# Kernel optimization log

Measured on AMD Instinct MI355X. Metric: run time of the kernel, lower is better.

Reference implementation:

```python
import jax, jax.numpy as jnp
import numpy as np

N_QUBITS = 10
N_LAYERS = 4
OUTPUT = 16
BATCH = 4096
DIM = 2 ** N_QUBITS  # 1024, amplitude-embedding dimension


def setup_inputs() -> dict:
    key = jax.random.key(0)
    k1, k2, k3, k4 = jax.random.split(key, 4)
    X = jax.random.normal(k1, (BATCH, DIM), jnp.float32)
    weights = jax.random.normal(k2, (N_LAYERS, N_QUBITS, 3), jnp.float32)  # StronglyEntanglingLayers params
    W = jax.random.normal(k3, (OUTPUT, N_QUBITS), jnp.float32) / np.sqrt(N_QUBITS)
    b = jax.random.normal(k4, (OUTPUT,), jnp.float32) * 0.01
    return {"X": X, "weights": weights, "W": W, "b": b}


def _rot_matrix(phi, theta, omega):
    # PennyLane Rot(phi, theta, omega) = RZ(omega) @ RY(theta) @ RZ(phi)
    c = jnp.cos(theta / 2).astype(jnp.complex64)
    s = jnp.sin(theta / 2).astype(jnp.complex64)
    a = jnp.exp(-0.5j * (phi + omega)) * c
    bq = -jnp.exp(0.5j * (phi - omega)) * s
    cq = jnp.exp(-0.5j * (phi - omega)) * s
    d = jnp.exp(0.5j * (phi + omega)) * c
    return jnp.stack([jnp.stack([a, bq]), jnp.stack([cq, d])])  # (2,2) complex64


def _apply_1q(state, U, q, n):
    # wire 0 is the most-significant bit (PennyLane default.qubit convention)
    A, B = 2 ** q, 2 ** (n - q - 1)
    s = state.reshape(-1, A, 2, B)
    s = jnp.einsum('ij,bajc->baic', U, s)
    return s.reshape(-1, 2 ** n)


def _cnot(state, c, t, n):
    hi, lo = (c, t) if c < t else (t, c)
    s = state.reshape(-1, 2 ** hi, 2, 2 ** (lo - hi - 1), 2, 2 ** (n - lo - 1))
    if c < t:
        # control axis 2, target axis 4
        s0 = s[:, :, 0]                      # (B, H, M, 2, L)
        s1 = jnp.flip(s[:, :, 1], axis=3)    # flip target where control=1
        s = jnp.stack([s0, s1], axis=2)
    else:
        # control axis 4, target axis 2
        s0 = s[:, :, :, :, 0, :]             # (B, H, 2, M, L)
        s1 = jnp.flip(s[:, :, :, :, 1, :], axis=2)
        s = jnp.stack([s0, s1], axis=4)
    return s.reshape(-1, 2 ** n)


def _circuit(X, weights):
    n = N_QUBITS
    # AmplitudeEmbedding (pad_with=0.0; here input dim == 2**n so just normalize)
    nrm = jnp.linalg.norm(X, axis=-1, keepdims=True)
    state = (X / nrm).astype(jnp.complex64)  # (B, 2**n)
    for l in range(N_LAYERS):
        for q in range(n):
            U = _rot_matrix(weights[l, q, 0], weights[l, q, 1], weights[l, q, 2])
            state = _apply_1q(state, U, q, n)
        r = (l % (n - 1)) + 1  # StronglyEntanglingLayers default imprimitive range
        for q in range(n):
            state = _cnot(state, q, (q + r) % n, n)
    probs = state.real ** 2 + state.imag ** 2  # (B, 2**n)
    # <Z_i> = sum_s probs[s] * (1 - 2*bit_i(s)); wire 0 = MSB
    idx = np.arange(2 ** n)
    bits = (idx[:, None] >> np.arange(n - 1, -1, -1)[None, :]) & 1  # (2**n, n)
    signs = jnp.asarray(1 - 2 * bits, jnp.float32)
    return probs @ signs  # (B, n)


def reference(X, weights, W, b):
    z = _circuit(X, weights)          # (B, n_qubits)
    return z @ W.T + b                # Linear head; nn.Tanh is defined but unused in forward
```

## Files before the change

kernel.cpp:

```cpp
#include <hip/hip_runtime.h>
#include <stdint.h>

#define NQ 10
#define DIMQ 1024
#define BATCH 4096

typedef float f32x2 __attribute__((ext_vector_type(2)));

__global__ __launch_bounds__(64) void prep_g(const float* __restrict__ wts,
                                             float* __restrict__ Gg) {
  int g = threadIdx.x;
  if (g < 40) {
    float phi = wts[g * 3 + 0], th = wts[g * 3 + 1], om = wts[g * 3 + 2];
    float ct = cosf(0.5f * th), s = sinf(0.5f * th);
    float ap = 0.5f * (phi + om), am = 0.5f * (phi - om);
    float cp = cosf(ap), spp = sinf(ap), cm = cosf(am), sm = sinf(am);
    float aR = ct * cp,  aI = -ct * spp;
    float bR = -s * cm,  bI = -s * sm;
    float cR = s * cm,   cI = -s * sm;
    float dR = ct * cp,  dI = ct * spp;
    float* o = Gg + g * 16;
    o[0]  = aR;  o[1]  = aR;  o[2]  = -aI; o[3]  = aI;
    o[4]  = bR;  o[5]  = bR;  o[6]  = -bI; o[7]  = bI;
    o[8]  = cR;  o[9]  = cR;  o[10] = -cI; o[11] = cI;
    o[12] = dR;  o[13] = dR;  o[14] = -dI; o[15] = dI;
  }
}

__host__ __device__ constexpr int cperm_c(int x, int r) {
  for (int q = 0; q < NQ; ++q) {
    const int c = 9 - q;
    int t = c - r; if (t < 0) t += NQ;
    x ^= ((x >> c) & 1) << t;
  }
  return x;
}
constexpr int amask(int q) {
  int a = 0;
  for (int b = 0; b < 6; ++b) a |= ((cperm_c(1 << b, 4) >> (9 - q)) & 1) << b;
  return a;
}
constexpr int mmask(int q) {
  int m = 0;
  for (int b = 0; b < 4; ++b) m |= ((cperm_c(1 << (6 + b), 4) >> (9 - q)) & 1) << b;
  return m;
}

__device__ __forceinline__ f32x2 swapv(f32x2 v) {
  return __builtin_shufflevector(v, v, 1, 0);
}

template<int CTRL>
__device__ __forceinline__ float dpp1(float x) {
  return __int_as_float(
      __builtin_amdgcn_update_dpp(0, __float_as_int(x), CTRL, 0xF, 0xF, true));
}
template<int P>
__device__ __forceinline__ float shufl(float x) {
  if constexpr (P == 0)      return dpp1<0xB1>(x);
  else if constexpr (P == 1) return dpp1<0x4E>(x);
  else if constexpr (P == 2) return dpp1<0x141>(dpp1<0x1B>(x));
  else if constexpr (P == 3) return dpp1<0x140>(dpp1<0x141>(x));
  else return __int_as_float(
      __builtin_amdgcn_ds_swizzle(__float_as_int(x), 0x401F));
}

template<int MT>
__device__ __forceinline__ void rotR(f32x2 (&s)[16], const f32x2* __restrict__ C) {
  const f32x2 C0 = C[0], C1 = C[1], C2 = C[2], C3 = C[3];
  const f32x2 C4 = C[4], C5 = C[5], C6 = C[6], C7 = C[7];
  #pragma unroll
  for (int e0 = 0; e0 < 16; ++e0) {
    if (e0 & MT) continue;
    const int e1 = e0 | MT;
    f32x2 x0 = s[e0], x1 = s[e1], w0 = swapv(x0), w1 = swapv(x1);
    s[e0] = C0 * x0 + C1 * w0 + C2 * x1 + C3 * w1;
    s[e1] = C4 * x0 + C5 * w0 + C6 * x1 + C7 * w1;
  }
}

template<int P>
__device__ __forceinline__ void rotL(f32x2 (&s)[16], const f32x2* __restrict__ C,
                                     int lane) {
  const int L = (lane >> P) & 1;
  const f32x2 A0 = L ? C[6] : C[0], A1 = L ? C[7] : C[1];
  const f32x2 B0 = L ? C[4] : C[2], B1 = L ? C[5] : C[3];
  #pragma unroll
  for (int e = 0; e < 16; ++e) {
    f32x2 o;
    o.x = shufl<P>(s[e].x);
    o.y = shufl<P>(s[e].y);
    s[e] = A0 * s[e] + A1 * swapv(s[e]) + B0 * o + B1 * swapv(o);
  }
}

__device__ __forceinline__ void rot5(f32x2 (&s)[16], const f32x2* __restrict__ C,
                                     int lane) {
  const int L = lane >> 5;
  const f32x2 A0 = L ? C[6] : C[0], A1 = L ? C[7] : C[1];
  const f32x2 B0 = L ? C[4] : C[2], B1 = L ? C[5] : C[3];
  #pragma unroll
  for (int e = 0; e < 16; ++e) {
    unsigned xr = __float_as_uint(s[e].x), xi = __float_as_uint(s[e].y);
    auto rr = __builtin_amdgcn_permlane32_swap(xr, xr, false, false);
    auto ri = __builtin_amdgcn_permlane32_swap(xi, xi, false, false);
    f32x2 o;
    o.x = __uint_as_float(L ? rr[0] : rr[1]);
    o.y = __uint_as_float(L ? ri[0] : ri[1]);
    s[e] = A0 * s[e] + A1 * swapv(s[e]) + B0 * o + B1 * swapv(o);
  }
}

template<int R>
__device__ __forceinline__ void perm_state(f32x2 (&s)[16], f32x2* __restrict__ L,
                                           int lane) {
  constexpr int K0=cperm_c(1,R),  K1=cperm_c(2,R),  K2=cperm_c(4,R),
                K3=cperm_c(8,R),  K4=cperm_c(16,R), K5=cperm_c(32,R),
                C6=cperm_c(64,R), C7=cperm_c(128,R),
                C8=cperm_c(256,R),C9=cperm_c(512,R);
  const int yl = ((lane & 1)  ? K0 : 0) ^ ((lane & 2)  ? K1 : 0) ^
                 ((lane & 4)  ? K2 : 0) ^ ((lane & 8)  ? K3 : 0) ^
                 ((lane & 16) ? K4 : 0) ^ ((lane & 32) ? K5 : 0);
  #pragma unroll
  for (int e = 0; e < 16; ++e) {
    const int ye = ((e & 1) ? C6 : 0) ^ ((e & 2) ? C7 : 0) ^
                   ((e & 4) ? C8 : 0) ^ ((e & 8) ? C9 : 0);
    L[yl ^ ye] = s[e];
  }
  #pragma unroll
  for (int e = 0; e < 16; ++e) s[e] = L[(e << 6) | lane];
}

__device__ __forceinline__ float red64(float v) {
  v += dpp1<0xB1>(v);
  v += dpp1<0x4E>(v);
  v += dpp1<0x141>(dpp1<0x1B>(v));
  v += dpp1<0x140>(dpp1<0x141>(v));
  v += __int_as_float(__builtin_amdgcn_ds_swizzle(__float_as_int(v), 0x401F));
  auto p = __builtin_amdgcn_permlane32_swap(__float_as_uint(v),
                                            __float_as_uint(v), false, false);
  return __uint_as_float(p[0]) + __uint_as_float(p[1]);
}

template<int LYR>
__device__ __forceinline__ void do_layer(f32x2 (&s)[16],
                                         const f32x2* __restrict__ Cq,
                                         f32x2* __restrict__ L, int lane) {
  const f32x2* G = Cq + LYR * 80;
  rotR<8>(s, G + 0);
  rotR<4>(s, G + 8);
  rotR<2>(s, G + 16);
  rotR<1>(s, G + 24);
  rot5   (s, G + 32, lane);
  rotL<4>(s, G + 40, lane);
  rotL<3>(s, G + 48, lane);
  rotL<2>(s, G + 56, lane);
  rotL<1>(s, G + 64, lane);
  rotL<0>(s, G + 72, lane);
  if constexpr (LYR < 3) perm_state<LYR + 1>(s, L, lane);
}

template<int M>
__device__ __forceinline__ void wht(float (&h)[16]) {
  #pragma unroll
  for (int e0 = 0; e0 < 16; ++e0) {
    if (e0 & M) continue;
    float u = h[e0], v = h[e0 | M];
    h[e0] = u + v;
    h[e0 | M] = u - v;
  }
}

template<int Q>
__device__ __forceinline__ float zfin(const float (&h)[16], int lane, float rn2) {
  constexpr int aq = amask(Q);
  constexpr int mq = mmask(Q);
  float t = h[mq];
  if constexpr (aq != 0) {
    int par = __builtin_popcount(lane & aq) & 1;
    t = par ? -t : t;
  }
  return red64(t) * rn2;
}

__global__ __launch_bounds__(256, 2) void vqc_sim(const float* __restrict__ X,
                                                  const float* __restrict__ Gg,
                                                  const float* __restrict__ W,
                                                  const float* __restrict__ bias,
                                                  float* __restrict__ out) {
  __shared__ f32x2 lds[4][DIMQ];
  const int lane = threadIdx.x & 63;
  const int w = threadIdx.x >> 6;
  const int row = blockIdx.x * 4 + w;
  f32x2* L = lds[w];
  const f32x2* Cq = (const f32x2*)Gg;

  f32x2 s[16];

  const float* xr = X + (size_t)row * DIMQ;
  float ss = 0.f;
  #pragma unroll
  for (int e = 0; e < 16; ++e) {
    s[e].x = xr[(e << 6) | lane];
    s[e].y = 0.f;
    ss += s[e].x * s[e].x;
  }
  const float rn2 = 1.0f / red64(ss);

  do_layer<0>(s, Cq, L, lane);
  do_layer<1>(s, Cq, L, lane);
  do_layer<2>(s, Cq, L, lane);
  do_layer<3>(s, Cq, L, lane);

  float h[16];
  #pragma unroll
  for (int e = 0; e < 16; ++e) h[e] = s[e].x * s[e].x + s[e].y * s[e].y;
  wht<1>(h); wht<2>(h); wht<4>(h); wht<8>(h);

  float z[10];
  z[0] = zfin<0>(h, lane, rn2);
  z[1] = zfin<1>(h, lane, rn2);
  z[2] = zfin<2>(h, lane, rn2);
  z[3] = zfin<3>(h, lane, rn2);
  z[4] = zfin<4>(h, lane, rn2);
  z[5] = zfin<5>(h, lane, rn2);
  z[6] = zfin<6>(h, lane, rn2);
  z[7] = zfin<7>(h, lane, rn2);
  z[8] = zfin<8>(h, lane, rn2);
  z[9] = zfin<9>(h, lane, rn2);

  if (lane < 16) {
    float acc = bias[lane];
    #pragma unroll
    for (int q = 0; q < 10; ++q) acc += z[q] * W[lane * 10 + q];
    out[(size_t)row * 16 + lane] = acc;
  }
}

extern "C" void kernel_launch(void* const* d_in, const int* in_sizes, int n_in,
                              void* d_out, int out_size, void* d_ws, size_t ws_size,
                              hipStream_t stream) {
  const float* X    = (const float*)d_in[0];
  const float* wts  = (const float*)d_in[1];
  const float* W    = (const float*)d_in[2];
  const float* bias = (const float*)d_in[3];
  float* out = (float*)d_out;
  float* Gg = (float*)d_ws;

  hipLaunchKernelGGL(prep_g,  dim3(1),         dim3(64),  0, stream, wts, Gg);
  hipLaunchKernelGGL(vqc_sim, dim3(BATCH / 4), dim3(256), 0, stream, X, Gg, W, bias, out);
}
```

Measured before the change: 103.2 us.

## Process two batch rows per wavefront and use permlane16 swap for lane-16 exchange

```diff
diff --git a/kernel.cpp b/kernel.cpp
--- a/kernel.cpp
+++ b/kernel.cpp
@@ -6,6 +6,12 @@
 #define BATCH 4096
 
 typedef float f32x2 __attribute__((ext_vector_type(2)));
+
+#if __has_builtin(__builtin_amdgcn_permlane16_swap)
+#define HAS_PL16 1
+#else
+#define HAS_PL16 0
+#endif
 
 __global__ __launch_bounds__(64) void prep_g(const float* __restrict__ wts,
                                              float* __restrict__ Gg) {
@@ -60,60 +66,102 @@
   if constexpr (P == 0)      return dpp1<0xB1>(x);
   else if constexpr (P == 1) return dpp1<0x4E>(x);
   else if constexpr (P == 2) return dpp1<0x141>(dpp1<0x1B>(x));
-  else if constexpr (P == 3) return dpp1<0x140>(dpp1<0x141>(x));
-  else return __int_as_float(
-      __builtin_amdgcn_ds_swizzle(__float_as_int(x), 0x401F));
+  else                       return dpp1<0x140>(dpp1<0x141>(x));
+}
+
+__device__ __forceinline__ float x16(float x, bool hi) {
+#if HAS_PL16
+  auto rr = __builtin_amdgcn_permlane16_swap(__float_as_uint(x),
+                                             __float_as_uint(x), false, false);
+  return __uint_as_float(hi ? rr[0] : rr[1]);
+#else
+  (void)hi;
+  return __int_as_float(__builtin_amdgcn_ds_swizzle(__float_as_int(x), 0x401F));
+#endif
+}
+
+__device__ __forceinline__ float red64(float v) {
+  v += dpp1<0xB1>(v);
+  v += dpp1<0x4E>(v);
+  v += dpp1<0x141>(dpp1<0x1B>(v));
+  v += dpp1<0x140>(dpp1<0x141>(v));
+#if HAS_PL16
+  { auto rr = __builtin_amdgcn_permlane16_swap(__float_as_uint(v),
+                                               __float_as_uint(v), false, false);
+    v = __uint_as_float(rr[0]) + __uint_as_float(rr[1]); }
+#else
+  v += __int_as_float(__builtin_amdgcn_ds_swizzle(__float_as_int(v), 0x401F));
+#endif
+  auto p = __builtin_amdgcn_permlane32_swap(__float_as_uint(v),
+                                            __float_as_uint(v), false, false);
+  return __uint_as_float(p[0]) + __uint_as_float(p[1]);
 }
 
 template<int MT>
-__device__ __forceinline__ void rotR(f32x2 (&s)[16], const f32x2* __restrict__ C) {
+__device__ __forceinline__ void rotR2(f32x2 (&s)[32], const f32x2* __restrict__ C) {
   const f32x2 C0 = C[0], C1 = C[1], C2 = C[2], C3 = C[3];
   const f32x2 C4 = C[4], C5 = C[5], C6 = C[6], C7 = C[7];
   #pragma unroll
-  for (int e0 = 0; e0 < 16; ++e0) {
-    if (e0 & MT) continue;
-    const int e1 = e0 | MT;
-    f32x2 x0 = s[e0], x1 = s[e1], w0 = swapv(x0), w1 = swapv(x1);
-    s[e0] = C0 * x0 + C1 * w0 + C2 * x1 + C3 * w1;
-    s[e1] = C4 * x0 + C5 * w0 + C6 * x1 + C7 * w1;
-  }
+  for (int g = 0; g < 32; g += 16)
+    #pragma unroll
+    for (int e0 = 0; e0 < 16; ++e0) {
+      if (e0 & MT) continue;
+      const int i0 = g + e0, i1 = g + (e0 | MT);
+      f32x2 x0 = s[i0], x1 = s[i1], w0 = swapv(x0), w1 = swapv(x1);
+      s[i0] = C0 * x0 + C1 * w0 + C2 * x1 + C3 * w1;
+      s[i1] = C4 * x0 + C5 * w0 + C6 * x1 + C7 * w1;
+    }
 }
 
 template<int P>
-__device__ __forceinline__ void rotL(f32x2 (&s)[16], const f32x2* __restrict__ C,
-                                     int lane) {
+__device__ __forceinline__ void rotL2(f32x2 (&s)[32], const f32x2* __restrict__ C,
+                                      int lane) {
   const int L = (lane >> P) & 1;
   const f32x2 A0 = L ? C[6] : C[0], A1 = L ? C[7] : C[1];
   const f32x2 B0 = L ? C[4] : C[2], B1 = L ? C[5] : C[3];
   #pragma unroll
-  for (int e = 0; e < 16; ++e) {
+  for (int i = 0; i < 32; ++i) {
     f32x2 o;
-    o.x = shufl<P>(s[e].x);
-    o.y = shufl<P>(s[e].y);
-    s[e] = A0 * s[e] + A1 * swapv(s[e]) + B0 * o + B1 * swapv(o);
-  }
-}
-
-__device__ __forceinline__ void rot5(f32x2 (&s)[16], const f32x2* __restrict__ C,
-                                     int lane) {
+    o.x = shufl<P>(s[i].x);
+    o.y = shufl<P>(s[i].y);
+    s[i] = A0 * s[i] + A1 * swapv(s[i]) + B0 * o + B1 * swapv(o);
+  }
+}
+
+__device__ __forceinline__ void rot16_2(f32x2 (&s)[32], const f32x2* __restrict__ C,
+                                        int lane) {
+  const bool H = (lane & 16) != 0;
+  const f32x2 A0 = H ? C[6] : C[0], A1 = H ? C[7] : C[1];
+  const f32x2 B0 = H ? C[4] : C[2], B1 = H ? C[5] : C[3];
+  #pragma unroll
+  for (int i = 0; i < 32; ++i) {
+    f32x2 o;
+    o.x = x16(s[i].x, H);
+    o.y = x16(s[i].y, H);
+    s[i] = A0 * s[i] + A1 * swapv(s[i]) + B0 * o + B1 * swapv(o);
+  }
+}
+
+__device__ __forceinline__ void rot5_2(f32x2 (&s)[32], const f32x2* __restrict__ C,
+                                       int lane) {
   const int L = lane >> 5;
   const f32x2 A0 = L ? C[6] : C[0], A1 = L ? C[7] : C[1];
   const f32x2 B0 = L ? C[4] : C[2], B1 = L ? C[5] : C[3];
   #pragma unroll
-  for (int e = 0; e < 16; ++e) {
-    unsigned xr = __float_as_uint(s[e].x), xi = __float_as_uint(s[e].y);
+  for (int i = 0; i < 32; ++i) {
+    unsigned xr = __float_as_uint(s[i].x), xi = __float_as_uint(s[i].y);
     auto rr = __builtin_amdgcn_permlane32_swap(xr, xr, false, false);
     auto ri = __builtin_amdgcn_permlane32_swap(xi, xi, false, false);
     f32x2 o;
     o.x = __uint_as_float(L ? rr[0] : rr[1]);
     o.y = __uint_as_float(L ? ri[0] : ri[1]);
-    s[e] = A0 * s[e] + A1 * swapv(s[e]) + B0 * o + B1 * swapv(o);
+    s[i] = A0 * s[i] + A1 * swapv(s[i]) + B0 * o + B1 * swapv(o);
   }
 }
 
 template<int R>
-__device__ __forceinline__ void perm_state(f32x2 (&s)[16], f32x2* __restrict__ L,
-                                           int lane) {
+__device__ __forceinline__ void perm2(f32x2 (&s)[32], f32x2* __restrict__ L0,
+                                      f32x2* __restrict__ L1, int lane) {
   constexpr int K0=cperm_c(1,R),  K1=cperm_c(2,R),  K2=cperm_c(4,R),
                 K3=cperm_c(8,R),  K4=cperm_c(16,R), K5=cperm_c(32,R),
                 C6=cperm_c(64,R), C7=cperm_c(128,R),
@@ -123,41 +171,16 @@
                  ((lane & 16) ? K4 : 0) ^ ((lane & 32) ? K5 : 0);
   #pragma unroll
   for (int e = 0; e < 16; ++e) {
-    const int ye = ((e & 1) ? C6 : 0) ^ ((e & 2) ? C7 : 0) ^
-                   ((e & 4) ? C8 : 0) ^ ((e & 8) ? C9 : 0);
-    L[yl ^ ye] = s[e];
-  }
-  #pragma unroll
-  for (int e = 0; e < 16; ++e) s[e] = L[(e << 6) | lane];
-}
-
-__device__ __forceinline__ float red64(float v) {
-  v += dpp1<0xB1>(v);
-  v += dpp1<0x4E>(v);
-  v += dpp1<0x141>(dpp1<0x1B>(v));
-  v += dpp1<0x140>(dpp1<0x141>(v));
-  v += __int_as_float(__builtin_amdgcn_ds_swizzle(__float_as_int(v), 0x401F));
-  auto p = __builtin_amdgcn_permlane32_swap(__float_as_uint(v),
-                                            __float_as_uint(v), false, false);
-  return __uint_as_float(p[0]) + __uint_as_float(p[1]);
-}
-
-template<int LYR>
-__device__ __forceinline__ void do_layer(f32x2 (&s)[16],
-                                         const f32x2* __restrict__ Cq,
-                                         f32x2* __restrict__ L, int lane) {
-  const f32x2* G = Cq + LYR * 80;
-  rotR<8>(s, G + 0);
-  rotR<4>(s, G + 8);
-  rotR<2>(s, G + 16);
-  rotR<1>(s, G + 24);
-  rot5   (s, G + 32, lane);
-  rotL<4>(s, G + 40, lane);
-  rotL<3>(s, G + 48, lane);
-  rotL<2>(s, G + 56, lane);
-  rotL<1>(s, G + 64, lane);
-  rotL<0>(s, G + 72, lane);
-  if constexpr (LYR < 3) perm_state<LYR + 1>(s, L, lane);
+    const int y = yl ^ (((e & 1) ? C6 : 0) ^ ((e & 2) ? C7 : 0) ^
+                        ((e & 4) ? C8 : 0) ^ ((e & 8) ? C9 : 0));
+    L0[y] = s[e];
+    L1[y] = s[16 + e];
+  }
+  #pragma unroll
+  for (int e = 0; e < 16; ++e) {
+    s[e]      = L0[(e << 6) | lane];
+    s[16 + e] = L1[(e << 6) | lane];
+  }
 }
 
 template<int M>
@@ -188,52 +211,77 @@
                                                   const float* __restrict__ W,
                                                   const float* __restrict__ bias,
                                                   float* __restrict__ out) {
-  __shared__ f32x2 lds[4][DIMQ];
+  __shared__ f32x2 lds[4][2][DIMQ];
   const int lane = threadIdx.x & 63;
   const int w = threadIdx.x >> 6;
-  const int row = blockIdx.x * 4 + w;
-  f32x2* L = lds[w];
+  const int row0 = (blockIdx.x * 4 + w) * 2;
+  f32x2* L0 = lds[w][0];
+  f32x2* L1 = lds[w][1];
   const f32x2* Cq = (const f32x2*)Gg;
 
-  f32x2 s[16];
-
-  const float* xr = X + (size_t)row * DIMQ;
-  float ss = 0.f;
-  #pragma unroll
-  for (int e = 0; e < 16; ++e) {
-    s[e].x = xr[(e << 6) | lane];
-    s[e].y = 0.f;
-    ss += s[e].x * s[e].x;
-  }
-  const float rn2 = 1.0f / red64(ss);
-
-  do_layer<0>(s, Cq, L, lane);
-  do_layer<1>(s, Cq, L, lane);
-  do_layer<2>(s, Cq, L, lane);
-  do_layer<3>(s, Cq, L, lane);
-
-  float h[16];
-  #pragma unroll
-  for (int e = 0; e < 16; ++e) h[e] = s[e].x * s[e].x + s[e].y * s[e].y;
-  wht<1>(h); wht<2>(h); wht<4>(h); wht<8>(h);
-
-  float z[10];
-  z[0] = zfin<0>(h, lane, rn2);
-  z[1] = zfin<1>(h, lane, rn2);
-  z[2] = zfin<2>(h, lane, rn2);
-  z[3] = zfin<3>(h, lane, rn2);
-  z[4] = zfin<4>(h, lane, rn2);
-  z[5] = zfin<5>(h, lane, rn2);
-  z[6] = zfin<6>(h, lane, rn2);
-  z[7] = zfin<7>(h, lane, rn2);
-  z[8] = zfin<8>(h, lane, rn2);
-  z[9] = zfin<9>(h, lane, rn2);
-
-  if (lane < 16) {
-    float acc = bias[lane];
+  f32x2 s[32];
+  float rn2[2];
+
+  const float* xr = X + (size_t)row0 * DIMQ;
+  #pragma unroll
+  for (int r = 0; r < 2; ++r) {
+    float ss = 0.f;
     #pragma unroll
-    for (int q = 0; q < 10; ++q) acc += z[q] * W[lane * 10 + q];
-    out[(size_t)row * 16 + lane] = acc;
+    for (int e = 0; e < 16; ++e) {
+      float v = xr[r * DIMQ + (e << 6) + lane];
+      s[r * 16 + e].x = v;
+      s[r * 16 + e].y = 0.f;
+      ss += v * v;
+    }
+    rn2[r] = 1.0f / red64(ss);
+  }
+
+  #pragma unroll 1
+  for (int l = 0; l < 4; ++l) {
+    const f32x2* G = Cq + l * 80;
+    rotR2<8>(s, G);
+    rotR2<4>(s, G + 8);
+    rotR2<2>(s, G + 16);
+    rotR2<1>(s, G + 24);
+    rot5_2 (s, G + 32, lane);
+    rot16_2(s, G + 40, lane);
+    rotL2<3>(s, G + 48, lane);
+    rotL2<2>(s, G + 56, lane);
+    rotL2<1>(s, G + 64, lane);
+    rotL2<0>(s, G + 72, lane);
+    if (l == 0)      perm2<1>(s, L0, L1, lane);
+    else if (l == 1) perm2<2>(s, L0, L1, lane);
+    else if (l == 2) perm2<3>(s, L0, L1, lane);
+  }
+
+  #pragma unroll
+  for (int r = 0; r < 2; ++r) {
+    float h[16];
+    #pragma unroll
+    for (int e = 0; e < 16; ++e) {
+      f32x2 t = s[r * 16 + e];
+      h[e] = t.x * t.x + t.y * t.y;
+    }
+    wht<1>(h); wht<2>(h); wht<4>(h); wht<8>(h);
+
+    float z[10];
+    z[0] = zfin<0>(h, lane, rn2[r]);
+    z[1] = zfin<1>(h, lane, rn2[r]);
+    z[2] = zfin<2>(h, lane, rn2[r]);
+    z[3] = zfin<3>(h, lane, rn2[r]);
+    z[4] = zfin<4>(h, lane, rn2[r]);
+    z[5] = zfin<5>(h, lane, rn2[r]);
+    z[6] = zfin<6>(h, lane, rn2[r]);
+    z[7] = zfin<7>(h, lane, rn2[r]);
+    z[8] = zfin<8>(h, lane, rn2[r]);
+    z[9] = zfin<9>(h, lane, rn2[r]);
+
+    if (lane < 16) {
+      float acc = bias[lane];
+      #pragma unroll
+      for (int q = 0; q < 10; ++q) acc += z[q] * W[lane * 10 + q];
+      out[(size_t)(row0 + r) * 16 + lane] = acc;
+    }
   }
 }
 
@@ -248,5 +296,5 @@
   float* Gg = (float*)d_ws;
 
   hipLaunchKernelGGL(prep_g,  dim3(1),         dim3(64),  0, stream, wts, Gg);
-  hipLaunchKernelGGL(vqc_sim, dim3(BATCH / 4), dim3(256), 0, stream, X, Gg, W, bias, out);
-}
+  hipLaunchKernelGGL(vqc_sim, dim3(BATCH / 8), dim3(256), 0, stream, X, Gg, W, bias, out);
+}
```

After: 108.9 us. 1.05x slower.

## Factor Rot gates into diagonal phase tables plus real RY rotations

Applied to the files above, without the earlier changes.

```diff
diff --git a/kernel.cpp b/kernel.cpp
--- a/kernel.cpp
+++ b/kernel.cpp
@@ -7,25 +7,11 @@
 
 typedef float f32x2 __attribute__((ext_vector_type(2)));
 
-__global__ __launch_bounds__(64) void prep_g(const float* __restrict__ wts,
-                                             float* __restrict__ Gg) {
-  int g = threadIdx.x;
-  if (g < 40) {
-    float phi = wts[g * 3 + 0], th = wts[g * 3 + 1], om = wts[g * 3 + 2];
-    float ct = cosf(0.5f * th), s = sinf(0.5f * th);
-    float ap = 0.5f * (phi + om), am = 0.5f * (phi - om);
-    float cp = cosf(ap), spp = sinf(ap), cm = cosf(am), sm = sinf(am);
-    float aR = ct * cp,  aI = -ct * spp;
-    float bR = -s * cm,  bI = -s * sm;
-    float cR = s * cm,   cI = -s * sm;
-    float dR = ct * cp,  dI = ct * spp;
-    float* o = Gg + g * 16;
-    o[0]  = aR;  o[1]  = aR;  o[2]  = -aI; o[3]  = aI;
-    o[4]  = bR;  o[5]  = bR;  o[6]  = -bI; o[7]  = bI;
-    o[8]  = cR;  o[9]  = cR;  o[10] = -cI; o[11] = cI;
-    o[12] = dR;  o[13] = dR;  o[14] = -dI; o[15] = dI;
-  }
-}
+#if __has_builtin(__builtin_amdgcn_permlane16_swap)
+#define HAS_PL16 1
+#else
+#define HAS_PL16 0
+#endif
 
 __host__ __device__ constexpr int cperm_c(int x, int r) {
   for (int q = 0; q < NQ; ++q) {
@@ -46,8 +32,33 @@
   return m;
 }
 
-__device__ __forceinline__ f32x2 swapv(f32x2 v) {
-  return __builtin_shufflevector(v, v, 1, 0);
+__global__ __launch_bounds__(64) void prep_g(const float* __restrict__ wts,
+                                             float* __restrict__ Gg) {
+  const int t = threadIdx.x;
+  if (t < 40) {
+    float th = wts[t * 3 + 1];
+    ((float2*)Gg)[t] = make_float2(cosf(0.5f * th), sinf(0.5f * th));
+  }
+  f32x2* D0 = (f32x2*)(Gg + 128);
+  f32x2* E  = D0 + 1024;
+  auto sphase = [&](int l, int i, int comp) {
+    float s = 0.f;
+    for (int q = 0; q < 10; ++q) {
+      float sg = ((i >> (9 - q)) & 1) ? 0.5f : -0.5f;
+      s += sg * wts[(l * 10 + q) * 3 + comp];
+    }
+    return s;
+  };
+  for (int k = 0; k < 16; ++k) {
+    int idx = (k << 6) | t;
+    float p0 = sphase(0, idx, 0);
+    D0[idx] = (f32x2){cosf(p0), sinf(p0)};
+    #pragma unroll 1
+    for (int l = 0; l < 3; ++l) {
+      float a = sphase(l, idx, 2) + sphase(l + 1, cperm_c(idx, l + 1), 0);
+      E[l * 1024 + idx] = (f32x2){cosf(a), sinf(a)};
+    }
+  }
 }
 
 template<int CTRL>
@@ -60,45 +71,76 @@
   if constexpr (P == 0)      return dpp1<0xB1>(x);
   else if constexpr (P == 1) return dpp1<0x4E>(x);
   else if constexpr (P == 2) return dpp1<0x141>(dpp1<0x1B>(x));
-  else if constexpr (P == 3) return dpp1<0x140>(dpp1<0x141>(x));
-  else return __int_as_float(
-      __builtin_amdgcn_ds_swizzle(__float_as_int(x), 0x401F));
+  else                       return dpp1<0x140>(dpp1<0x141>(x));
+}
+__device__ __forceinline__ float x16(float x, bool hi) {
+#if HAS_PL16
+  auto rr = __builtin_amdgcn_permlane16_swap(__float_as_uint(x),
+                                             __float_as_uint(x), false, false);
+  return __uint_as_float(hi ? rr[0] : rr[1]);
+#else
+  (void)hi;
+  return __int_as_float(__builtin_amdgcn_ds_swizzle(__float_as_int(x), 0x401F));
+#endif
+}
+
+__device__ __forceinline__ float red64(float v) {
+  v += dpp1<0xB1>(v);
+  v += dpp1<0x4E>(v);
+  v += dpp1<0x141>(dpp1<0x1B>(v));
+  v += dpp1<0x140>(dpp1<0x141>(v));
+#if HAS_PL16
+  { auto rr = __builtin_amdgcn_permlane16_swap(__float_as_uint(v),
+                                               __float_as_uint(v), false, false);
+    v = __uint_as_float(rr[0]) + __uint_as_float(rr[1]); }
+#else
+  v += __int_as_float(__builtin_amdgcn_ds_swizzle(__float_as_int(v), 0x401F));
+#endif
+  auto p = __builtin_amdgcn_permlane32_swap(__float_as_uint(v),
+                                            __float_as_uint(v), false, false);
+  return __uint_as_float(p[0]) + __uint_as_float(p[1]);
 }
 
 template<int MT>
-__device__ __forceinline__ void rotR(f32x2 (&s)[16], const f32x2* __restrict__ C) {
-  const f32x2 C0 = C[0], C1 = C[1], C2 = C[2], C3 = C[3];
-  const f32x2 C4 = C[4], C5 = C[5], C6 = C[6], C7 = C[7];
+__device__ __forceinline__ void ry_reg(f32x2 (&s)[16], float2 cs) {
+  const float c = cs.x, sn = cs.y;
   #pragma unroll
   for (int e0 = 0; e0 < 16; ++e0) {
     if (e0 & MT) continue;
     const int e1 = e0 | MT;
-    f32x2 x0 = s[e0], x1 = s[e1], w0 = swapv(x0), w1 = swapv(x1);
-    s[e0] = C0 * x0 + C1 * w0 + C2 * x1 + C3 * w1;
-    s[e1] = C4 * x0 + C5 * w0 + C6 * x1 + C7 * w1;
-  }
-}
-
+    f32x2 x0 = s[e0], x1 = s[e1];
+    s[e0] = c * x0 - sn * x1;
+    s[e1] = sn * x0 + c * x1;
+  }
+}
 template<int P>
-__device__ __forceinline__ void rotL(f32x2 (&s)[16], const f32x2* __restrict__ C,
-                                     int lane) {
-  const int L = (lane >> P) & 1;
-  const f32x2 A0 = L ? C[6] : C[0], A1 = L ? C[7] : C[1];
-  const f32x2 B0 = L ? C[4] : C[2], B1 = L ? C[5] : C[3];
+__device__ __forceinline__ void ry_dpp(f32x2 (&s)[16], float2 cs, int lane) {
+  const float c = cs.x;
+  const float ss = ((lane >> P) & 1) ? cs.y : -cs.y;
   #pragma unroll
   for (int e = 0; e < 16; ++e) {
     f32x2 o;
     o.x = shufl<P>(s[e].x);
     o.y = shufl<P>(s[e].y);
-    s[e] = A0 * s[e] + A1 * swapv(s[e]) + B0 * o + B1 * swapv(o);
-  }
-}
-
-__device__ __forceinline__ void rot5(f32x2 (&s)[16], const f32x2* __restrict__ C,
-                                     int lane) {
+    s[e] = c * s[e] + ss * o;
+  }
+}
+__device__ __forceinline__ void ry16(f32x2 (&s)[16], float2 cs, int lane) {
+  const bool H = (lane & 16) != 0;
+  const float c = cs.x;
+  const float ss = H ? cs.y : -cs.y;
+  #pragma unroll
+  for (int e = 0; e < 16; ++e) {
+    f32x2 o;
+    o.x = x16(s[e].x, H);
+    o.y = x16(s[e].y, H);
+    s[e] = c * s[e] + ss * o;
+  }
+}
+__device__ __forceinline__ void ry5(f32x2 (&s)[16], float2 cs, int lane) {
   const int L = lane >> 5;
-  const f32x2 A0 = L ? C[6] : C[0], A1 = L ? C[7] : C[1];
-  const f32x2 B0 = L ? C[4] : C[2], B1 = L ? C[5] : C[3];
+  const float c = cs.x;
+  const float ss = L ? cs.y : -cs.y;
   #pragma unroll
   for (int e = 0; e < 16; ++e) {
     unsigned xr = __float_as_uint(s[e].x), xi = __float_as_uint(s[e].y);
@@ -107,7 +149,19 @@
     f32x2 o;
     o.x = __uint_as_float(L ? rr[0] : rr[1]);
     o.y = __uint_as_float(L ? ri[0] : ri[1]);
-    s[e] = A0 * s[e] + A1 * swapv(s[e]) + B0 * o + B1 * swapv(o);
+    s[e] = c * s[e] + ss * o;
+  }
+}
+
+__device__ __forceinline__ void emul(f32x2 (&s)[16], const f32x2* __restrict__ E,
+                                     int lane) {
+  #pragma unroll
+  for (int e = 0; e < 16; ++e) {
+    f32x2 t = E[(e << 6) | lane];
+    f32x2 r;
+    r.x = s[e].x * t.x - s[e].y * t.y;
+    r.y = s[e].x * t.y + s[e].y * t.x;
+    s[e] = r;
   }
 }
 
@@ -131,33 +185,26 @@
   for (int e = 0; e < 16; ++e) s[e] = L[(e << 6) | lane];
 }
 
-__device__ __forceinline__ float red64(float v) {
-  v += dpp1<0xB1>(v);
-  v += dpp1<0x4E>(v);
-  v += dpp1<0x141>(dpp1<0x1B>(v));
-  v += dpp1<0x140>(dpp1<0x141>(v));
-  v += __int_as_float(__builtin_amdgcn_ds_swizzle(__float_as_int(v), 0x401F));
-  auto p = __builtin_amdgcn_permlane32_swap(__float_as_uint(v),
-                                            __float_as_uint(v), false, false);
-  return __uint_as_float(p[0]) + __uint_as_float(p[1]);
-}
-
 template<int LYR>
 __device__ __forceinline__ void do_layer(f32x2 (&s)[16],
-                                         const f32x2* __restrict__ Cq,
+                                         const float2* __restrict__ ryc,
+                                         const f32x2* __restrict__ Etab,
                                          f32x2* __restrict__ L, int lane) {
-  const f32x2* G = Cq + LYR * 80;
-  rotR<8>(s, G + 0);
-  rotR<4>(s, G + 8);
-  rotR<2>(s, G + 16);
-  rotR<1>(s, G + 24);
-  rot5   (s, G + 32, lane);
-  rotL<4>(s, G + 40, lane);
-  rotL<3>(s, G + 48, lane);
-  rotL<2>(s, G + 56, lane);
-  rotL<1>(s, G + 64, lane);
-  rotL<0>(s, G + 72, lane);
-  if constexpr (LYR < 3) perm_state<LYR + 1>(s, L, lane);
+  const float2* G = ryc + LYR * 10;
+  ry_reg<8>(s, G[0]);
+  ry_reg<4>(s, G[1]);
+  ry_reg<2>(s, G[2]);
+  ry_reg<1>(s, G[3]);
+  ry5     (s, G[4], lane);
+  ry16    (s, G[5], lane);
+  ry_dpp<3>(s, G[6], lane);
+  ry_dpp<2>(s, G[7], lane);
+  ry_dpp<1>(s, G[8], lane);
+  ry_dpp<0>(s, G[9], lane);
+  if constexpr (LYR < 3) {
+    emul(s, Etab + LYR * 1024, lane);
+    perm_state<LYR + 1>(s, L, lane);
+  }
 }
 
 template<int M>
@@ -170,7 +217,6 @@
     h[e0 | M] = u - v;
   }
 }
-
 template<int Q>
 __device__ __forceinline__ float zfin(const float (&h)[16], int lane, float rn2) {
   constexpr int aq = amask(Q);
@@ -193,7 +239,9 @@
   const int w = threadIdx.x >> 6;
   const int row = blockIdx.x * 4 + w;
   f32x2* L = lds[w];
-  const f32x2* Cq = (const f32x2*)Gg;
+  const float2* ryc = (const float2*)Gg;
+  const f32x2* D0   = (const f32x2*)(Gg + 128);
+  const f32x2* Etab = D0 + 1024;
 
   f32x2 s[16];
 
@@ -201,16 +249,16 @@
   float ss = 0.f;
   #pragma unroll
   for (int e = 0; e < 16; ++e) {
-    s[e].x = xr[(e << 6) | lane];
-    s[e].y = 0.f;
-    ss += s[e].x * s[e].x;
+    float v = xr[(e << 6) | lane];
+    ss += v * v;
+    s[e] = v * D0[(e << 6) | lane];
   }
   const float rn2 = 1.0f / red64(ss);
 
-  do_layer<0>(s, Cq, L, lane);
-  do_layer<1>(s, Cq, L, lane);
-  do_layer<2>(s, Cq, L, lane);
-  do_layer<3>(s, Cq, L, lane);
+  do_layer<0>(s, ryc, Etab, L, lane);
+  do_layer<1>(s, ryc, Etab, L, lane);
+  do_layer<2>(s, ryc, Etab, L, lane);
+  do_layer<3>(s, ryc, Etab, L, lane);
 
   float h[16];
   #pragma unroll
```

Measured after the change: 118.6 us. 1.15x slower.
